# Kernel optimization log

Measured on AMD Instinct MI355X. Metric: run time of the kernel, lower is better.

The kernel has to match this reference:

```python
import jax, jax.numpy as jnp
import numpy as np

B, S, D, H = 4, 2048, 1024, 16
HD = D // H


def setup_inputs() -> dict:
    key = jax.random.key(0)
    ks = jax.random.split(key, 11)
    sc = 0.02
    return {
        "q": jax.random.normal(ks[0], (B, S, D), jnp.float32),
        "k": jax.random.normal(ks[1], (B, S, D), jnp.float32),
        "v": jax.random.normal(ks[2], (B, S, D), jnp.float32),
        "wq_w": jax.random.normal(ks[3], (D, D), jnp.float32) * sc,
        "wq_b": jax.random.normal(ks[4], (D,), jnp.float32) * sc,
        "wk_w": jax.random.normal(ks[5], (D, D), jnp.float32) * sc,
        "wk_b": jax.random.normal(ks[6], (D,), jnp.float32) * sc,
        "wv_w": jax.random.normal(ks[7], (D, D), jnp.float32) * sc,
        "wv_b": jax.random.normal(ks[8], (D,), jnp.float32) * sc,
        "wo_w": jax.random.normal(ks[9], (D, D), jnp.float32) * sc,
        "wo_b": jax.random.normal(ks[10], (D,), jnp.float32) * sc,
    }


def _heads(x):
    # [B,S,D] -> [B,H,S,HD]
    return x.reshape(B, S, H, HD).transpose(0, 2, 1, 3)


def reference(q, k, v, wq_w, wq_b, wk_w, wk_b, wv_w, wv_b, wo_w, wo_b):
    # nn.Linear: y = x @ W^T + b
    Q = _heads(q @ wq_w.T + wq_b)
    K = _heads(k @ wk_w.T + wk_b)
    V = _heads(v @ wv_w.T + wv_b)
    scale = 1.0 / jnp.sqrt(jnp.float32(HD))
    scores = jnp.einsum("bhqd,bhkd->bhqk", Q, K) * scale
    weights = jax.nn.softmax(scores, axis=-1)  # dropout p=0 -> identity
    ctx = jnp.einsum("bhqk,bhkd->bhqd", weights, V)  # [B,H,S,HD]
    merged = ctx.transpose(0, 2, 1, 3).reshape(B, S, D)
    out = merged @ wo_w.T + wo_b
    return out, ctx
```

## Files before the change

### kernel.cpp

```cpp
#include <hip/hip_runtime.h>
#include <hip/hip_bf16.h>

#define HDD 64
#define NH 16
#define SEQ 2048
#define DM 1024
#define BB 4

using bf16x8 = __attribute__((ext_vector_type(8))) short;
using floatx4 = __attribute__((ext_vector_type(4))) float;
typedef unsigned int u32;

__device__ __forceinline__ short f2bf(float f) {
    __hip_bfloat16 h = __float2bfloat16(f);
    union { __hip_bfloat16 h; short s; } c;
    c.h = h;
    return c.s;
}

__device__ __forceinline__ void stage8f(short* dst, const float* s) {
    float4 a = *(const float4*)s;
    float4 b = *(const float4*)(s + 4);
    bf16x8 r;
    r[0] = f2bf(a.x); r[1] = f2bf(a.y); r[2] = f2bf(a.z); r[3] = f2bf(a.w);
    r[4] = f2bf(b.x); r[5] = f2bf(b.y); r[6] = f2bf(b.z); r[7] = f2bf(b.w);
    *(bf16x8*)dst = r;
}

__global__ __launch_bounds__(256) void proj_kernel(
    const float* __restrict__ q, const float* __restrict__ k, const float* __restrict__ v,
    const float* __restrict__ wq, const float* __restrict__ bq,
    const float* __restrict__ wk, const float* __restrict__ bk,
    const float* __restrict__ wv, const float* __restrict__ bv,
    short* __restrict__ Qh, short* __restrict__ Kh, short* __restrict__ Vh)
{
    const int z = blockIdx.z;
    const float* X  = (z == 0) ? q  : (z == 1) ? k  : v;
    const float* W  = (z == 0) ? wq : (z == 1) ? wk : wv;
    const float* Bp = (z == 0) ? bq : (z == 1) ? bk : bv;
    short* Dst      = (z == 0) ? Qh : (z == 1) ? Kh : Vh;
    const float qscale = (z == 0) ? (0.125f * 1.44269504088896f) : 1.0f;

    const int m0 = blockIdx.x * 128;
    const int n0 = blockIdx.y * 128;
    const int tid = threadIdx.x;
    const int w = tid >> 6, lane = tid & 63, lc = lane & 15, lq = lane >> 4;
    const int wm = w >> 1, wn = w & 1;

    __shared__ alignas(16) short As[128 * 40];
    __shared__ alignas(16) short Bs[128 * 40];

    floatx4 acc[4][4];
#pragma unroll
    for (int i = 0; i < 4; i++)
#pragma unroll
        for (int j = 0; j < 4; j++) acc[i][j] = floatx4{0.f, 0.f, 0.f, 0.f};

    for (int kt = 0; kt < DM / 32; ++kt) {
        __syncthreads();
#pragma unroll
        for (int c = 0; c < 2; ++c) {
            int chunk = c * 256 + tid;
            int row = chunk >> 2;
            int col = (chunk & 3) * 8;
            stage8f(As + row * 40 + col, X + (size_t)(m0 + row) * DM + kt * 32 + col);
            stage8f(Bs + row * 40 + col, W + (size_t)(n0 + row) * DM + kt * 32 + col);
        }
        __syncthreads();

        bf16x8 aF[4], bF[4];
#pragma unroll
        for (int i = 0; i < 4; i++)
            aF[i] = *(const bf16x8*)(As + (wm * 64 + i * 16 + lc) * 40 + lq * 8);
#pragma unroll
        for (int j = 0; j < 4; j++)
            bF[j] = *(const bf16x8*)(Bs + (wn * 64 + j * 16 + lc) * 40 + lq * 8);
        __builtin_amdgcn_s_setprio(1);
#pragma unroll
        for (int i = 0; i < 4; i++)
#pragma unroll
            for (int j = 0; j < 4; j++)
                acc[i][j] = __builtin_amdgcn_mfma_f32_16x16x32_bf16(aF[i], bF[j], acc[i][j], 0, 0, 0);
        __builtin_amdgcn_s_setprio(0);
    }

#pragma unroll
    for (int j = 0; j < 4; j++) {
        int n = n0 + wn * 64 + j * 16 + lc;
        float bias = Bp[n];
        int h = n >> 6, hd = n & 63;
#pragma unroll
        for (int i = 0; i < 4; i++) {
#pragma unroll
            for (int r = 0; r < 4; r++) {
                int m = m0 + wm * 64 + i * 16 + lq * 4 + r;
                int b = m >> 11, s = m & 2047;
                float val = (acc[i][j][r] + bias) * qscale;
                Dst[(((size_t)(b * NH + h)) * SEQ + s) * HDD + hd] = f2bf(val);
            }
        }
    }
}

__global__ __launch_bounds__(256) void attn_kernel(
    const short* __restrict__ Qh, const short* __restrict__ Kh,
    const short* __restrict__ Vh, float* __restrict__ ctxout)
{
    const int linear = blockIdx.y * 32 + blockIdx.x;
    const int swz = (linear & 7) * 256 + (linear >> 3);
    const int qb = swz & 31;
    const int bh = swz >> 5;

    const int tid = threadIdx.x;
    const int w = tid >> 6, lane = tid & 63, lc = lane & 15, lq = lane >> 4;
    const int qbase = qb * 64 + w * 16;

    const short* Qp = Qh + (size_t)bh * SEQ * HDD;
    const short* Kp = Kh + (size_t)bh * SEQ * HDD;
    const short* Vp = Vh + (size_t)bh * SEQ * HDD;

    __shared__ alignas(16) short Vt[2][64 * 72];

    bf16x8 aQ[2];
#pragma unroll
    for (int f = 0; f < 2; ++f)
        aQ[f] = *(const bf16x8*)(Qp + (size_t)(qbase + lc) * HDD + f * 32 + lq * 8);

    float mOld = -1e30f, lSum = 0.f;
    floatx4 accO[4];
#pragma unroll
    for (int dt = 0; dt < 4; dt++) accO[dt] = floatx4{0.f, 0.f, 0.f, 0.f};

    const int kv2 = (tid >> 3) * 2;
    const int d0 = (tid & 7) * 8;
    const int swzb = (tid & 7) << 3;
    const int kvs_w = kv2 ^ swzb;

    {
        bf16x8 v0 = *(const bf16x8*)(Vp + (size_t)kv2 * HDD + d0);
        bf16x8 v1 = *(const bf16x8*)(Vp + (size_t)(kv2 + 1) * HDD + d0);
#pragma unroll
        for (int i = 0; i < 8; i++) {
            u32 pk = ((u32)(unsigned short)v0[i]) | (((u32)(unsigned short)v1[i]) << 16);
            *(u32*)(&Vt[0][(d0 + i) * 72 + kvs_w]) = pk;
        }
    }
    __syncthreads();

    const int NT = SEQ / 64;
    for (int kt = 0; kt < NT; ++kt) {
        const int cur = kt & 1;
        const int kv0 = kt * 64;

        bf16x8 nv0{}, nv1{};
        const bool have = (kt + 1 < NT);
        if (have) {
            const short* nvp = Vp + (size_t)(kv0 + 64 + kv2) * HDD + d0;
            nv0 = *(const bf16x8*)nvp;
            nv1 = *(const bf16x8*)(nvp + HDD);
        }

        floatx4 sc[4];
        __builtin_amdgcn_s_setprio(1);
#pragma unroll
        for (int nt = 0; nt < 4; nt++) {
            floatx4 sv = floatx4{0.f, 0.f, 0.f, 0.f};
#pragma unroll
            for (int f = 0; f < 2; f++) {
                bf16x8 bK = *(const bf16x8*)(Kp + (size_t)(kv0 + nt * 16 + lc) * HDD + f * 32 + lq * 8);
                sv = __builtin_amdgcn_mfma_f32_16x16x32_bf16(bK, aQ[f], sv, 0, 0, 0);
            }
            sc[nt] = sv;
        }
        __builtin_amdgcn_s_setprio(0);

        float mx = sc[0][0];
#pragma unroll
        for (int nt = 0; nt < 4; nt++)
#pragma unroll
            for (int r = 0; r < 4; r++) mx = fmaxf(mx, sc[nt][r]);
        mx = fmaxf(mx, __shfl_xor(mx, 16, 64));
        mx = fmaxf(mx, __shfl_xor(mx, 32, 64));
        const float mNew = fmaxf(mOld, mx);
        const float alpha = __builtin_amdgcn_exp2f(mOld - mNew);
        float rsum = 0.f;
#pragma unroll
        for (int nt = 0; nt < 4; nt++)
#pragma unroll
            for (int r = 0; r < 4; r++) {
                float p = __builtin_amdgcn_exp2f(sc[nt][r] - mNew);
                sc[nt][r] = p;
                rsum += p;
            }
        rsum += __shfl_xor(rsum, 16, 64);
        rsum += __shfl_xor(rsum, 32, 64);
        lSum = lSum * alpha + rsum;
        mOld = mNew;

#pragma unroll
        for (int dt = 0; dt < 4; dt++)
#pragma unroll
            for (int r = 0; r < 4; r++) accO[dt][r] *= alpha;

        u32 pw[4][2];
#pragma unroll
        for (int nt = 0; nt < 4; nt++) {
            pw[nt][0] = ((u32)(unsigned short)f2bf(sc[nt][0])) |
                        (((u32)(unsigned short)f2bf(sc[nt][1])) << 16);
            pw[nt][1] = ((u32)(unsigned short)f2bf(sc[nt][2])) |
                        (((u32)(unsigned short)f2bf(sc[nt][3])) << 16);
        }
        const int srcA = ((lq & 1) << 5) + lc;
        const int srcB = srcA + 16;
        const bool selHi = (lq >> 1) != 0;

#pragma unroll
        for (int f = 0; f < 2; f++) {
            u32 a0 = (u32)__shfl((int)pw[2 * f][0], srcA, 64);
            u32 a1 = (u32)__shfl((int)pw[2 * f][1], srcA, 64);
            u32 a2 = (u32)__shfl((int)pw[2 * f][0], srcB, 64);
            u32 a3 = (u32)__shfl((int)pw[2 * f][1], srcB, 64);
            u32 b0 = (u32)__shfl((int)pw[2 * f + 1][0], srcA, 64);
            u32 b1 = (u32)__shfl((int)pw[2 * f + 1][1], srcA, 64);
            u32 b2 = (u32)__shfl((int)pw[2 * f + 1][0], srcB, 64);
            u32 b3 = (u32)__shfl((int)pw[2 * f + 1][1], srcB, 64);
            union { u32 u[4]; bf16x8 v; } P;
            P.u[0] = selHi ? b0 : a0;
            P.u[1] = selHi ? b1 : a1;
            P.u[2] = selHi ? b2 : a2;
            P.u[3] = selHi ? b3 : a3;
            __builtin_amdgcn_s_setprio(1);
#pragma unroll
            for (int dt = 0; dt < 4; dt++) {
                const int d = dt * 16 + lc;
                const int kvs = (f * 32 + lq * 8) ^ (((d >> 3) & 7) << 3);
                bf16x8 bV = *(const bf16x8*)(&Vt[cur][d * 72 + kvs]);
                accO[dt] = __builtin_amdgcn_mfma_f32_16x16x32_bf16(bV, P.v, accO[dt], 0, 0, 0);
            }
            __builtin_amdgcn_s_setprio(0);
        }

        if (have) {
            short* dstb = &Vt[cur ^ 1][0];
#pragma unroll
            for (int i = 0; i < 8; i++) {
                u32 pk = ((u32)(unsigned short)nv0[i]) | (((u32)(unsigned short)nv1[i]) << 16);
                *(u32*)(dstb + (d0 + i) * 72 + kvs_w) = pk;
            }
        }
        __syncthreads();
    }

    const float inv = 1.0f / lSum;
    float* orow = ctxout + ((size_t)bh * SEQ + qbase + lc) * HDD;
#pragma unroll
    for (int dt = 0; dt < 4; dt++) {
        float4 st;
        st.x = accO[dt][0] * inv;
        st.y = accO[dt][1] * inv;
        st.z = accO[dt][2] * inv;
        st.w = accO[dt][3] * inv;
        *(float4*)(orow + dt * 16 + lq * 4) = st;
    }
}

__global__ __launch_bounds__(256) void outproj_kernel(
    const float* __restrict__ ctxb, const float* __restrict__ wo,
    const float* __restrict__ bo, float* __restrict__ out)
{
    const int m0 = blockIdx.x * 128;
    const int n0 = blockIdx.y * 128;
    const int tid = threadIdx.x;
    const int w = tid >> 6, lane = tid & 63, lc = lane & 15, lq = lane >> 4;
    const int wm = w >> 1, wn = w & 1;

    __shared__ alignas(16) short As[128 * 40];
    __shared__ alignas(16) short Bs[128 * 40];

    floatx4 acc[4][4];
#pragma unroll
    for (int i = 0; i < 4; i++)
#pragma unroll
        for (int j = 0; j < 4; j++) acc[i][j] = floatx4{0.f, 0.f, 0.f, 0.f};

    for (int kt = 0; kt < DM / 32; ++kt) {
        __syncthreads();
#pragma unroll
        for (int c = 0; c < 2; ++c) {
            int chunk = c * 256 + tid;
            int row = chunk >> 2;
            int col = (chunk & 3) * 8;
            int m = m0 + row;
            int b = m >> 11, s = m & 2047;
            int kcol = kt * 32 + col;
            int h = kcol >> 6, hd = kcol & 63;
            stage8f(As + row * 40 + col,
                    ctxb + (((size_t)(b * NH + h)) * SEQ + s) * HDD + hd);
            stage8f(Bs + row * 40 + col, wo + (size_t)(n0 + row) * DM + kt * 32 + col);
        }
        __syncthreads();

        bf16x8 aF[4], bF[4];
#pragma unroll
        for (int i = 0; i < 4; i++)
            aF[i] = *(const bf16x8*)(As + (wm * 64 + i * 16 + lc) * 40 + lq * 8);
#pragma unroll
        for (int j = 0; j < 4; j++)
            bF[j] = *(const bf16x8*)(Bs + (wn * 64 + j * 16 + lc) * 40 + lq * 8);
        __builtin_amdgcn_s_setprio(1);
#pragma unroll
        for (int i = 0; i < 4; i++)
#pragma unroll
            for (int j = 0; j < 4; j++)
                acc[i][j] = __builtin_amdgcn_mfma_f32_16x16x32_bf16(aF[i], bF[j], acc[i][j], 0, 0, 0);
        __builtin_amdgcn_s_setprio(0);
    }

#pragma unroll
    for (int j = 0; j < 4; j++) {
        int n = n0 + wn * 64 + j * 16 + lc;
        float bias = bo[n];
#pragma unroll
        for (int i = 0; i < 4; i++) {
#pragma unroll
            for (int r = 0; r < 4; r++) {
                int m = m0 + wm * 64 + i * 16 + lq * 4 + r;
                out[(size_t)m * DM + n] = acc[i][j][r] + bias;
            }
        }
    }
}

extern "C" void kernel_launch(void* const* d_in, const int* in_sizes, int n_in,
                              void* d_out, int out_size, void* d_ws, size_t ws_size,
                              hipStream_t stream) {
    const float* q  = (const float*)d_in[0];
    const float* k  = (const float*)d_in[1];
    const float* v  = (const float*)d_in[2];
    const float* wq = (const float*)d_in[3];
    const float* bq = (const float*)d_in[4];
    const float* wk = (const float*)d_in[5];
    const float* bk = (const float*)d_in[6];
    const float* wv = (const float*)d_in[7];
    const float* bv = (const float*)d_in[8];
    const float* wo = (const float*)d_in[9];
    const float* bo = (const float*)d_in[10];

    float* out0 = (float*)d_out;
    float* ctx  = out0 + (size_t)BB * SEQ * DM;

    short* Qh = (short*)d_ws;
    short* Kh = Qh + (size_t)BB * NH * SEQ * HDD;
    short* Vh = Kh + (size_t)BB * NH * SEQ * HDD;

    proj_kernel<<<dim3(64, 8, 3), 256, 0, stream>>>(q, k, v, wq, bq, wk, bk, wv, bv, Qh, Kh, Vh);
    attn_kernel<<<dim3(32, 64), 256, 0, stream>>>(Qh, Kh, Vh, ctx);
    outproj_kernel<<<dim3(64, 8), 256, 0, stream>>>(ctx, wo, bo, out0);
}
```

Baseline: 581.7 us.

## Pre-convert weights to bf16, emit bf16 ctx, widen attention blocks, lazy rescale

Adds a small kernel that converts all four weight matrices to bf16 once per call, so the projection GEMMs load bf16 weights directly instead of converting them per tile. The attention kernel now also writes a bf16 copy of ctx, which the output projection reads in place of the fp32 ctx, halving that traffic. Attention blocks grow to 512 threads covering 128 queries, with V staging split into 4-element pieces. The online softmax skips the rescale unless the running max rises by more than 8, saving multiplies at some risk to numerical range.

```diff
diff --git a/kernel.cpp b/kernel.cpp
--- a/kernel.cpp
+++ b/kernel.cpp
@@ -8,6 +8,7 @@
 #define BB 4
 
 using bf16x8 = __attribute__((ext_vector_type(8))) short;
+using bf16x4 = __attribute__((ext_vector_type(4))) short;
 using floatx4 = __attribute__((ext_vector_type(4))) float;
 typedef unsigned int u32;
 
@@ -27,18 +28,31 @@
     *(bf16x8*)dst = r;
 }
 
+__global__ __launch_bounds__(256) void wconv_kernel(
+    const float* __restrict__ w0, const float* __restrict__ w1,
+    const float* __restrict__ w2, const float* __restrict__ w3,
+    short* __restrict__ o0, short* __restrict__ o1,
+    short* __restrict__ o2, short* __restrict__ o3)
+{
+    const int z = blockIdx.y;
+    const float* src = (z == 0) ? w0 : (z == 1) ? w1 : (z == 2) ? w2 : w3;
+    short* dst       = (z == 0) ? o0 : (z == 1) ? o1 : (z == 2) ? o2 : o3;
+    size_t i = ((size_t)blockIdx.x * 256 + threadIdx.x) * 8;
+    stage8f(dst + i, src + i);
+}
+
 __global__ __launch_bounds__(256) void proj_kernel(
     const float* __restrict__ q, const float* __restrict__ k, const float* __restrict__ v,
-    const float* __restrict__ wq, const float* __restrict__ bq,
-    const float* __restrict__ wk, const float* __restrict__ bk,
-    const float* __restrict__ wv, const float* __restrict__ bv,
+    const short* __restrict__ wqb, const float* __restrict__ bq,
+    const short* __restrict__ wkb, const float* __restrict__ bk,
+    const short* __restrict__ wvb, const float* __restrict__ bv,
     short* __restrict__ Qh, short* __restrict__ Kh, short* __restrict__ Vh)
 {
     const int z = blockIdx.z;
-    const float* X  = (z == 0) ? q  : (z == 1) ? k  : v;
-    const float* W  = (z == 0) ? wq : (z == 1) ? wk : wv;
-    const float* Bp = (z == 0) ? bq : (z == 1) ? bk : bv;
-    short* Dst      = (z == 0) ? Qh : (z == 1) ? Kh : Vh;
+    const float* X  = (z == 0) ? q   : (z == 1) ? k   : v;
+    const short* Wb = (z == 0) ? wqb : (z == 1) ? wkb : wvb;
+    const float* Bp = (z == 0) ? bq  : (z == 1) ? bk  : bv;
+    short* Dst      = (z == 0) ? Qh  : (z == 1) ? Kh  : Vh;
     const float qscale = (z == 0) ? (0.125f * 1.44269504088896f) : 1.0f;
 
     const int m0 = blockIdx.x * 128;
@@ -64,7 +78,8 @@
             int row = chunk >> 2;
             int col = (chunk & 3) * 8;
             stage8f(As + row * 40 + col, X + (size_t)(m0 + row) * DM + kt * 32 + col);
-            stage8f(Bs + row * 40 + col, W + (size_t)(n0 + row) * DM + kt * 32 + col);
+            *(bf16x8*)(Bs + row * 40 + col) =
+                *(const bf16x8*)(Wb + (size_t)(n0 + row) * DM + kt * 32 + col);
         }
         __syncthreads();
 
@@ -102,18 +117,19 @@
     }
 }
 
-__global__ __launch_bounds__(256) void attn_kernel(
+__global__ __launch_bounds__(512) void attn_kernel(
     const short* __restrict__ Qh, const short* __restrict__ Kh,
-    const short* __restrict__ Vh, float* __restrict__ ctxout)
+    const short* __restrict__ Vh, float* __restrict__ ctxout,
+    short* __restrict__ ctxb)
 {
-    const int linear = blockIdx.y * 32 + blockIdx.x;
-    const int swz = (linear & 7) * 256 + (linear >> 3);
-    const int qb = swz & 31;
-    const int bh = swz >> 5;
+    const int linear = blockIdx.y * 16 + blockIdx.x;
+    const int swz = (linear & 7) * 128 + (linear >> 3);
+    const int qb = swz & 15;
+    const int bh = swz >> 4;
 
     const int tid = threadIdx.x;
     const int w = tid >> 6, lane = tid & 63, lc = lane & 15, lq = lane >> 4;
-    const int qbase = qb * 64 + w * 16;
+    const int qbase = qb * 128 + w * 16;
 
     const short* Qp = Qh + (size_t)bh * SEQ * HDD;
     const short* Kp = Kh + (size_t)bh * SEQ * HDD;
@@ -131,16 +147,17 @@
 #pragma unroll
     for (int dt = 0; dt < 4; dt++) accO[dt] = floatx4{0.f, 0.f, 0.f, 0.f};
 
-    const int kv2 = (tid >> 3) * 2;
-    const int d0 = (tid & 7) * 8;
-    const int swzb = (tid & 7) << 3;
+    const int kv2 = (tid >> 4) * 2;
+    const int d0 = (tid & 15) * 4;
+    const int swzb = ((d0 >> 3) & 7) << 3;
     const int kvs_w = kv2 ^ swzb;
 
     {
-        bf16x8 v0 = *(const bf16x8*)(Vp + (size_t)kv2 * HDD + d0);
-        bf16x8 v1 = *(const bf16x8*)(Vp + (size_t)(kv2 + 1) * HDD + d0);
-#pragma unroll
-        for (int i = 0; i < 8; i++) {
+        const short* vp = Vp + (size_t)kv2 * HDD + d0;
+        bf16x4 v0 = *(const bf16x4*)vp;
+        bf16x4 v1 = *(const bf16x4*)(vp + HDD);
+#pragma unroll
+        for (int i = 0; i < 4; i++) {
             u32 pk = ((u32)(unsigned short)v0[i]) | (((u32)(unsigned short)v1[i]) << 16);
             *(u32*)(&Vt[0][(d0 + i) * 72 + kvs_w]) = pk;
         }
@@ -152,12 +169,12 @@
         const int cur = kt & 1;
         const int kv0 = kt * 64;
 
-        bf16x8 nv0{}, nv1{};
+        bf16x4 nv0{}, nv1{};
         const bool have = (kt + 1 < NT);
         if (have) {
             const short* nvp = Vp + (size_t)(kv0 + 64 + kv2) * HDD + d0;
-            nv0 = *(const bf16x8*)nvp;
-            nv1 = *(const bf16x8*)(nvp + HDD);
+            nv0 = *(const bf16x4*)nvp;
+            nv1 = *(const bf16x4*)(nvp + HDD);
         }
 
         floatx4 sc[4];
@@ -181,26 +198,28 @@
             for (int r = 0; r < 4; r++) mx = fmaxf(mx, sc[nt][r]);
         mx = fmaxf(mx, __shfl_xor(mx, 16, 64));
         mx = fmaxf(mx, __shfl_xor(mx, 32, 64));
-        const float mNew = fmaxf(mOld, mx);
-        const float alpha = __builtin_amdgcn_exp2f(mOld - mNew);
+        if (!__all(mx - mOld <= 8.0f)) {
+            const float mNew = fmaxf(mOld, mx);
+            const float alpha = __builtin_amdgcn_exp2f(mOld - mNew);
+            lSum *= alpha;
+#pragma unroll
+            for (int dt = 0; dt < 4; dt++)
+#pragma unroll
+                for (int r = 0; r < 4; r++) accO[dt][r] *= alpha;
+            mOld = mNew;
+        }
         float rsum = 0.f;
 #pragma unroll
         for (int nt = 0; nt < 4; nt++)
 #pragma unroll
             for (int r = 0; r < 4; r++) {
-                float p = __builtin_amdgcn_exp2f(sc[nt][r] - mNew);
+                float p = __builtin_amdgcn_exp2f(sc[nt][r] - mOld);
                 sc[nt][r] = p;
                 rsum += p;
             }
         rsum += __shfl_xor(rsum, 16, 64);
         rsum += __shfl_xor(rsum, 32, 64);
-        lSum = lSum * alpha + rsum;
-        mOld = mNew;
-
-#pragma unroll
-        for (int dt = 0; dt < 4; dt++)
-#pragma unroll
-            for (int r = 0; r < 4; r++) accO[dt][r] *= alpha;
+        lSum += rsum;
 
         u32 pw[4][2];
 #pragma unroll
@@ -243,7 +262,7 @@
         if (have) {
             short* dstb = &Vt[cur ^ 1][0];
 #pragma unroll
-            for (int i = 0; i < 8; i++) {
+            for (int i = 0; i < 4; i++) {
                 u32 pk = ((u32)(unsigned short)nv0[i]) | (((u32)(unsigned short)nv1[i]) << 16);
                 *(u32*)(dstb + (d0 + i) * 72 + kvs_w) = pk;
             }
@@ -252,7 +271,9 @@
     }
 
     const float inv = 1.0f / lSum;
-    float* orow = ctxout + ((size_t)bh * SEQ + qbase + lc) * HDD;
+    const size_t rowoff = ((size_t)bh * SEQ + qbase + lc) * HDD;
+    float* orow = ctxout + rowoff;
+    short* brow = ctxb + rowoff;
 #pragma unroll
     for (int dt = 0; dt < 4; dt++) {
         float4 st;
@@ -261,11 +282,15 @@
         st.z = accO[dt][2] * inv;
         st.w = accO[dt][3] * inv;
         *(float4*)(orow + dt * 16 + lq * 4) = st;
+        uint2 bb;
+        bb.x = ((u32)(unsigned short)f2bf(st.x)) | (((u32)(unsigned short)f2bf(st.y)) << 16);
+        bb.y = ((u32)(unsigned short)f2bf(st.z)) | (((u32)(unsigned short)f2bf(st.w)) << 16);
+        *(uint2*)(brow + dt * 16 + lq * 4) = bb;
     }
 }
 
 __global__ __launch_bounds__(256) void outproj_kernel(
-    const float* __restrict__ ctxb, const float* __restrict__ wo,
+    const short* __restrict__ ctxb, const short* __restrict__ wob,
     const float* __restrict__ bo, float* __restrict__ out)
 {
     const int m0 = blockIdx.x * 128;
@@ -294,9 +319,10 @@
             int b = m >> 11, s = m & 2047;
             int kcol = kt * 32 + col;
             int h = kcol >> 6, hd = kcol & 63;
-            stage8f(As + row * 40 + col,
-                    ctxb + (((size_t)(b * NH + h)) * SEQ + s) * HDD + hd);
-            stage8f(Bs + row * 40 + col, wo + (size_t)(n0 + row) * DM + kt * 32 + col);
+            *(bf16x8*)(As + row * 40 + col) =
+                *(const bf16x8*)(ctxb + (((size_t)(b * NH + h)) * SEQ + s) * HDD + hd);
+            *(bf16x8*)(Bs + row * 40 + col) =
+                *(const bf16x8*)(wob + (size_t)(n0 + row) * DM + kt * 32 + col);
         }
         __syncthreads();
 
@@ -349,11 +375,18 @@
     float* out0 = (float*)d_out;
     float* ctx  = out0 + (size_t)BB * SEQ * DM;
 
-    short* Qh = (short*)d_ws;
-    short* Kh = Qh + (size_t)BB * NH * SEQ * HDD;
-    short* Vh = Kh + (size_t)BB * NH * SEQ * HDD;
-
-    proj_kernel<<<dim3(64, 8, 3), 256, 0, stream>>>(q, k, v, wq, bq, wk, bk, wv, bv, Qh, Kh, Vh);
-    attn_kernel<<<dim3(32, 64), 256, 0, stream>>>(Qh, Kh, Vh, ctx);
-    outproj_kernel<<<dim3(64, 8), 256, 0, stream>>>(ctx, wo, bo, out0);
-}
+    const size_t NELEM = (size_t)BB * NH * SEQ * HDD;
+    short* Qh   = (short*)d_ws;
+    short* Kh   = Qh + NELEM;
+    short* Vh   = Kh + NELEM;
+    short* ctxb = Vh + NELEM;
+    short* Wqb  = ctxb + NELEM;
+    short* Wkb  = Wqb + (size_t)DM * DM;
+    short* Wvb  = Wkb + (size_t)DM * DM;
+    short* Wob  = Wvb + (size_t)DM * DM;
+
+    wconv_kernel<<<dim3(512, 4), 256, 0, stream>>>(wq, wk, wv, wo, Wqb, Wkb, Wvb, Wob);
+    proj_kernel<<<dim3(64, 8, 3), 256, 0, stream>>>(q, k, v, Wqb, bq, Wkb, bk, Wvb, bv, Qh, Kh, Vh);
+    attn_kernel<<<dim3(16, 64), 512, 0, stream>>>(Qh, Kh, Vh, ctx, ctxb);
+    outproj_kernel<<<dim3(64, 8), 256, 0, stream>>>(ctxb, Wob, bo, out0);
+}
```

Result: faster. 561.0 us (-3.6%).
